# Performance work log

Measured on AMD Instinct MI355X. Metric: run time of the kernel, lower is better.

The kernel has to match this reference:

```python
import jax, jax.numpy as jnp
import numpy as np

N_VARS = 16
BATCH = 16
SEQ = 512
P = N_VARS * (N_VARS - 1)  # ordered pairs i != j


def setup_inputs() -> dict:
    key = jax.random.key(0)
    ks = jax.random.split(key, 12)
    n = N_VARS

    def w(k, shape, fan_in):
        return jax.random.normal(k, shape, dtype=jnp.float32) / np.sqrt(fan_in)

    z = lambda *s: jnp.zeros(s, jnp.float32)
    return {
        'data': jax.random.normal(ks[0], (BATCH, SEQ, n), dtype=jnp.float32),
        # structure learner: n*n -> 256 -> 128 -> n*n (dropout skipped / eval mode)
        'Ws1': w(ks[1], (n * n, 256), n * n), 'bs1': z(256),
        'Ws2': w(ks[2], (256, 128), 256), 'bs2': z(128),
        'Ws3': w(ks[3], (128, n * n), 128), 'bs3': z(n * n),
        # per-variable causal mechanisms (stacked): (n-1) -> 128 -> 64 -> 1
        'Wm1': w(ks[4], (n, n - 1, 128), n - 1), 'bm1': z(n, 128),
        'Wm2': w(ks[5], (n, 128, 64), 128), 'bm2': z(n, 64),
        'Wm3': w(ks[6], (n, 64), 64), 'bm3': z(n),
        # per-pair independence tests (stacked): 2 -> 32 -> 1, sigmoid
        'Wt1': w(ks[7], (P, 2, 32), 2), 'bt1': z(P, 32),
        'Wt2': w(ks[8], (P, 32), 32), 'bt2': z(P),
    }


def reference(data, Ws1, bs1, Ws2, bs2, Ws3, bs3,
              Wm1, bm1, Wm2, bm2, Wm3, bm3,
              Wt1, bt1, Wt2, bt2):
    B, S, n = data.shape
    N = B * S
    flat = data.reshape(N, n)  # [N, n] all samples

    # ---- correlations of batch-averaged series (vectorized corrcoef) ----
    avg = data.mean(axis=0)                    # [S, n]
    xc = avg - avg.mean(axis=0, keepdims=True)
    cov = xc.T @ xc                            # [n, n]
    std = jnp.sqrt(jnp.clip(jnp.diag(cov), 0.0))
    denom = std[:, None] * std[None, :]
    corr = jnp.abs(jnp.where(denom > 0, cov / jnp.where(denom > 0, denom, 1.0), 0.0))
    corr = corr * (1.0 - jnp.eye(n, dtype=corr.dtype))  # zero diagonal (i != j only)

    # ---- structure learner MLP -> sigmoid -> strict upper-tri DAG mask ----
    h = jax.nn.relu(corr.reshape(1, -1) @ Ws1 + bs1)
    h = jax.nn.relu(h @ Ws2 + bs2)
    adj = jax.nn.sigmoid(h @ Ws3 + bs3).reshape(n, n)
    adj = jnp.triu(adj, 1)

    # ---- causal mechanisms: gather-parents -> per-var MLP -> scatter ----
    idx = np.stack([[j for j in range(n) if j != v] for v in range(n)])  # [n, n-1]
    pmask = adj > 0.5
    parent_mask = pmask[idx, np.arange(n)[:, None]].astype(flat.dtype)   # [n, n-1]
    inp = flat[:, idx] * parent_mask[None]                               # [N, n, n-1]
    h1 = jax.nn.relu(jnp.einsum('nvp,vph->nvh', inp, Wm1) + bm1)         # [N, n, 128]
    h2 = jax.nn.relu(jnp.einsum('nvh,vhk->nvk', h1, Wm2) + bm2)          # [N, n, 64]
    mech = jnp.einsum('nvk,vk->nv', h2, Wm3) + bm3                       # [N, n]
    has_parents = parent_mask.sum(axis=1) > 0                            # [n]
    predictions = jnp.where(has_parents[None, :], mech, flat).reshape(B, S, n)

    # ---- batched per-pair independence tests ----
    pairs = np.array([(i, j) for i in range(n) for j in range(n) if i != j])
    pi, pj = pairs[:, 0], pairs[:, 1]
    X = jnp.stack([flat[:, pi], flat[:, pj]], axis=-1)                   # [N, P, 2]
    ht = jax.nn.relu(jnp.einsum('npc,pch->nph', X, Wt1) + bt1)           # [N, P, 32]
    s = jax.nn.sigmoid(jnp.einsum('nph,ph->np', ht, Wt2) + bt2).mean(axis=0)  # [P]
    scores = jnp.zeros((n, n), flat.dtype).at[pi, pj].set(s)

    return adj, predictions, scores
```

## Files before the change

### kernel.cpp

```cpp
#include <hip/hip_runtime.h>
#include <hip/hip_bf16.h>


typedef __attribute__((ext_vector_type(8))) short bf16x8;
typedef __attribute__((ext_vector_type(4))) short bf16x4;
typedef __attribute__((ext_vector_type(4))) float f32x4;

#define DEV __device__ __forceinline__
DEV short f2bf(float f){ __hip_bfloat16 h = __float2bfloat16(f); short s; __builtin_memcpy(&s,&h,2); return s; }

struct GraphSm {
    float avT[16 * 532];
    float part[512];
    float cov[256];
    float corr[256];
    float h1[256];
    float h2[128];
    float adj[256];
    float m[16];
    float stdv[16];
};
struct MechSm {
    short W2T[64 * 136];
    short H1[8][16 * 136];
    float W1[16 * 128];
    float B1[128];
    float B2[64];
    float W3[64];
};
struct PairSm {
    float w0[32], w1[32], bb[32], w2[32];
    float red[512];
    float b2s;
};
union SmU { GraphSm g; MechSm m; PairSm p; };

__global__ void __launch_bounds__(512, 2) k_fused(
    const float* __restrict__ data,
    const float* __restrict__ Ws1, const float* __restrict__ bs1,
    const float* __restrict__ Ws2, const float* __restrict__ bs2,
    const float* __restrict__ Ws3, const float* __restrict__ bs3,
    const float* __restrict__ Wm1, const float* __restrict__ bm1,
    const float* __restrict__ Wm2, const float* __restrict__ bm2,
    const float* __restrict__ Wm3, const float* __restrict__ bm3,
    const float* __restrict__ Wt1, const float* __restrict__ bt1,
    const float* __restrict__ Wt2, const float* __restrict__ bt2,
    float* __restrict__ out)
{
    __shared__ __align__(16) SmU sm;
    __shared__ float pm_s[16];
    __shared__ float hp_s;
    int tid = threadIdx.x, bid = blockIdx.x;

    if (bid >= 64) {
        int p = bid - 64;
        int i = p / 15, jr = p % 15;
        int j = jr + (jr >= i ? 1 : 0);
        if (tid < 32) {
            sm.p.w0[tid] = Wt1[p*64 + tid];
            sm.p.w1[tid] = Wt1[p*64 + 32 + tid];
            sm.p.bb[tid] = bt1[p*32 + tid];
            sm.p.w2[tid] = Wt2[p*32 + tid];
        }
        if (tid == 0) sm.p.b2s = bt2[p];
        __syncthreads();
        float b2sv = sm.p.b2s;
        float acc = 0.f;
        for (int it = 0; it < 16; ++it) {
            int s = it*512 + tid;
            float xa = data[s*16 + i];
            float xb = data[s*16 + j];
            float za = 0.f, zb = 0.f;
            #pragma unroll
            for (int h = 0; h < 32; h += 2) {
                float t1 = fmaf(xa, sm.p.w0[h],   fmaf(xb, sm.p.w1[h],   sm.p.bb[h]));
                za = fmaf(fmaxf(t1, 0.f), sm.p.w2[h],   za);
                float t2 = fmaf(xa, sm.p.w0[h+1], fmaf(xb, sm.p.w1[h+1], sm.p.bb[h+1]));
                zb = fmaf(fmaxf(t2, 0.f), sm.p.w2[h+1], zb);
            }
            float z = b2sv + za + zb;
            acc += __builtin_amdgcn_rcpf(1.f + __expf(-z));
        }
        sm.p.red[tid] = acc;
        __syncthreads();
        for (int off = 256; off > 0; off >>= 1) {
            if (tid < off) sm.p.red[tid] += sm.p.red[tid + off];
            __syncthreads();
        }
        if (tid == 0) out[256 + 131072 + i*16 + j] = sm.p.red[0] * (1.f/8192.f);
        return;
    }

    int v = bid >> 2, chunk = bid & 3;
    int gs0 = chunk * 2048;

    {
        int vb = (tid & 3) * 4, sg = tid >> 2;
        for (int k = 0; k < 4; ++k) {
            int s = sg + k*128;
            float ax=0.f, ay=0.f, az=0.f, aw=0.f;
            #pragma unroll
            for (int b = 0; b < 16; ++b) {
                float4 d4 = *(const float4*)&data[b*8192 + s*16 + vb];
                ax += d4.x; ay += d4.y; az += d4.z; aw += d4.w;
            }
            sm.g.avT[(vb+0)*532 + s] = ax * 0.0625f;
            sm.g.avT[(vb+1)*532 + s] = ay * 0.0625f;
            sm.g.avT[(vb+2)*532 + s] = az * 0.0625f;
            sm.g.avT[(vb+3)*532 + s] = aw * 0.0625f;
        }
    }
    __syncthreads();
    if (tid < 128) {
        int vv = tid >> 3, sgm = tid & 7;
        const float* rp = &sm.g.avT[vv*532 + sgm*64];
        float a0=0.f, a1=0.f, a2=0.f, a3=0.f;
        for (int s = 0; s < 64; s += 4) {
            float4 fa = *(const float4*)&rp[s];
            a0 += fa.x; a1 += fa.y; a2 += fa.z; a3 += fa.w;
        }
        sm.g.part[tid] = (a0+a1)+(a2+a3);
    }
    __syncthreads();
    if (tid < 16) {
        float ms = 0.f;
        #pragma unroll
        for (int q = 0; q < 8; ++q) ms += sm.g.part[tid*8 + q];
        sm.g.m[tid] = ms * (1.f/512.f);
    }
    __syncthreads();
    {
        int t = tid & 255, hh = tid >> 8;
        int ci = t >> 4, cj = t & 15;
        const float* pi_ = &sm.g.avT[ci*532 + hh*256];
        const float* pj_ = &sm.g.avT[cj*532 + hh*256];
        float a0=0.f, a1=0.f, a2=0.f, a3=0.f;
        for (int s = 0; s < 256; s += 4) {
            float4 fa = *(const float4*)&pi_[s];
            float4 fb = *(const float4*)&pj_[s];
            a0 = fmaf(fa.x, fb.x, a0); a1 = fmaf(fa.y, fb.y, a1);
            a2 = fmaf(fa.z, fb.z, a2); a3 = fmaf(fa.w, fb.w, a3);
        }
        sm.g.part[tid] = (a0+a1)+(a2+a3);
    }
    __syncthreads();
    if (tid < 256) {
        int ci = tid >> 4, cj = tid & 15;
        sm.g.cov[tid] = sm.g.part[tid] + sm.g.part[256 + tid]
                      - 512.f * sm.g.m[ci] * sm.g.m[cj];
    }
    __syncthreads();
    if (tid < 16) sm.g.stdv[tid] = sqrtf(fmaxf(sm.g.cov[tid*17], 0.f));
    __syncthreads();
    if (tid < 256) {
        int ci = tid >> 4, cj = tid & 15;
        float den = sm.g.stdv[ci] * sm.g.stdv[cj];
        sm.g.corr[tid] = (den > 0.f && ci != cj) ? fabsf(sm.g.cov[tid]/den) : 0.f;
    }
    __syncthreads();
    {
        int t = tid & 255, half = tid >> 8;
        const float* W1p = Ws1 + half*128*256;
        const float* cp  = sm.g.corr + half*128;
        float a0=0.f, a1=0.f, a2=0.f, a3=0.f;
        #pragma unroll 8
        for (int i = 0; i < 128; i += 4) {
            a0 = fmaf(cp[i  ], W1p[(i  )*256 + t], a0);
            a1 = fmaf(cp[i+1], W1p[(i+1)*256 + t], a1);
            a2 = fmaf(cp[i+2], W1p[(i+2)*256 + t], a2);
            a3 = fmaf(cp[i+3], W1p[(i+3)*256 + t], a3);
        }
        sm.g.part[half*256 + t] = (a0+a1)+(a2+a3);
    }
    __syncthreads();
    if (tid < 256) sm.g.h1[tid] = fmaxf(sm.g.part[tid] + sm.g.part[256+tid] + bs1[tid], 0.f);
    __syncthreads();
    {
        int t = tid & 127, qq = tid >> 7;
        const float* W2p = Ws2 + qq*64*128;
        const float* h1p = sm.g.h1 + qq*64;
        float a0=0.f, a1=0.f, a2=0.f, a3=0.f;
        #pragma unroll 4
        for (int i = 0; i < 64; i += 4) {
            a0 = fmaf(h1p[i  ], W2p[(i  )*128 + t], a0);
            a1 = fmaf(h1p[i+1], W2p[(i+1)*128 + t], a1);
            a2 = fmaf(h1p[i+2], W2p[(i+2)*128 + t], a2);
            a3 = fmaf(h1p[i+3], W2p[(i+3)*128 + t], a3);
        }
        sm.g.part[qq*128 + t] = (a0+a1)+(a2+a3);
    }
    __syncthreads();
    if (tid < 128)
        sm.g.h2[tid] = fmaxf(sm.g.part[tid] + sm.g.part[128+tid] + sm.g.part[256+tid]
                             + sm.g.part[384+tid] + bs2[tid], 0.f);
    __syncthreads();
    {
        int t = tid & 255, half = tid >> 8;
        const float* W3p = Ws3 + half*64*256;
        const float* h2p = sm.g.h2 + half*64;
        float a0=0.f, a1=0.f, a2=0.f, a3=0.f;
        #pragma unroll 4
        for (int i = 0; i < 64; i += 4) {
            a0 = fmaf(h2p[i  ], W3p[(i  )*256 + t], a0);
            a1 = fmaf(h2p[i+1], W3p[(i+1)*256 + t], a1);
            a2 = fmaf(h2p[i+2], W3p[(i+2)*256 + t], a2);
            a3 = fmaf(h2p[i+3], W3p[(i+3)*256 + t], a3);
        }
        sm.g.part[half*256 + t] = (a0+a1)+(a2+a3);
    }
    __syncthreads();
    if (tid < 256) {
        float z = sm.g.part[tid] + sm.g.part[256 + tid] + bs3[tid];
        float a = 1.f / (1.f + expf(-z));
        int r = tid >> 4, cc = tid & 15;
        float adjv = (r < cc) ? a : 0.f;
        sm.g.adj[tid] = adjv;
        if (bid == 0) out[tid] = adjv;
    }
    __syncthreads();
    if (tid < 15) {
        int jj = tid + (tid >= v ? 1 : 0);
        pm_s[tid] = (sm.g.adj[jj*16 + v] > 0.5f) ? 1.f : 0.f;
    }
    if (bid == 0 && tid >= 16 && tid < 32)
        out[256 + 131072 + (tid-16)*17] = 0.f;
    __syncthreads();
    if (tid == 0) {
        float s = 0.f;
        #pragma unroll
        for (int pr = 0; pr < 15; ++pr) s += pm_s[pr];
        hp_s = (s > 0.f) ? 1.f : 0.f;
    }
    __syncthreads();

    for (int e = tid; e < 2048; e += 512) {
        int k = e >> 7, h = e & 127;
        float val = 0.f;
        if (k != v) {
            int p = k - (k > v ? 1 : 0);
            val = Wm1[v*1920 + p*128 + h] * pm_s[p];
        }
        sm.m.W1[e] = val;
    }
    for (int e = tid; e < 8192; e += 512) {
        int h = e >> 6, jj2 = e & 63;
        sm.m.W2T[jj2*136 + h] = f2bf(Wm2[v*8192 + e]);
    }
    if (tid < 128) sm.m.B1[tid] = bm1[v*128 + tid];
    else if (tid < 192) sm.m.B2[tid - 128] = bm2[v*64 + tid - 128];
    else if (tid < 256) sm.m.W3[tid - 192] = Wm3[v*64 + tid - 192];
    __syncthreads();

    int lane = tid & 63, wid = tid >> 6;
    int c = lane & 15, q = lane >> 4;
    float hp = hp_s;
    float bm3v = bm3[v];

    bf16x8 a1f[8];
    #pragma unroll
    for (int ht = 0; ht < 8; ++ht) {
        #pragma unroll
        for (int jj = 0; jj < 8; ++jj) {
            int k = q*8 + jj;
            float w = (k < 16) ? sm.m.W1[k*128 + ht*16 + c] : 0.f;
            a1f[ht][jj] = f2bf(w);
        }
    }
    bf16x8 b2r[16];
    #pragma unroll
    for (int jt = 0; jt < 4; ++jt)
        #pragma unroll
        for (int ks = 0; ks < 4; ++ks)
            b2r[jt*4 + ks] = *(const bf16x8*)&sm.m.W2T[(jt*16 + c)*136 + ks*32 + q*8];
    float w3c[4], b2c[4];
    #pragma unroll
    for (int jt = 0; jt < 4; ++jt) { w3c[jt] = sm.m.W3[jt*16 + c]; b2c[jt] = sm.m.B2[jt*16 + c]; }

    short* h1buf = sm.m.H1[wid];

    for (int stl = 0; stl < 16; ++stl) {
        int st = wid*16 + stl;
        bf16x8 xb;
        #pragma unroll
        for (int i2 = 0; i2 < 8; ++i2) xb[i2] = 0;
        if (q < 2) {
            const float* xp = &data[(gs0 + st*16 + c)*16 + q*8];
            float4 u0 = *(const float4*)xp;
            float4 u1 = *(const float4*)(xp + 4);
            xb[0] = f2bf(u0.x); xb[1] = f2bf(u0.y);
            xb[2] = f2bf(u0.z); xb[3] = f2bf(u0.w);
            xb[4] = f2bf(u1.x); xb[5] = f2bf(u1.y);
            xb[6] = f2bf(u1.z); xb[7] = f2bf(u1.w);
        }
        f32x4 c1[8];
        #pragma unroll
        for (int ht = 0; ht < 8; ++ht) c1[ht] = *(const f32x4*)&sm.m.B1[ht*16 + q*4];
        #pragma unroll
        for (int ht = 0; ht < 8; ++ht)
            c1[ht] = __builtin_amdgcn_mfma_f32_16x16x32_bf16(a1f[ht], xb, c1[ht], 0, 0, 0);
        #pragma unroll
        for (int ht = 0; ht < 8; ++ht) {
            bf16x4 pk;
            #pragma unroll
            for (int r = 0; r < 4; ++r) pk[r] = f2bf(fmaxf(c1[ht][r], 0.f));
            *(bf16x4*)&h1buf[c*136 + ht*16 + q*4] = pk;
        }
        f32x4 c2[4];
        #pragma unroll
        for (int jt = 0; jt < 4; ++jt) {
            float bi = b2c[jt];
            c2[jt] = (f32x4){bi, bi, bi, bi};
        }
        #pragma unroll
        for (int ks = 0; ks < 4; ++ks) {
            bf16x8 a2 = *(const bf16x8*)&h1buf[c*136 + ks*32 + q*8];
            #pragma unroll
            for (int jt = 0; jt < 4; ++jt)
                c2[jt] = __builtin_amdgcn_mfma_f32_16x16x32_bf16(a2, b2r[jt*4 + ks], c2[jt], 0, 0, 0);
        }
        float part[4];
        #pragma unroll
        for (int r = 0; r < 4; ++r) part[r] = 0.f;
        #pragma unroll
        for (int jt = 0; jt < 4; ++jt)
            #pragma unroll
            for (int r = 0; r < 4; ++r)
                part[r] = fmaf(fmaxf(c2[jt][r], 0.f), w3c[jt], part[r]);
        #pragma unroll
        for (int off = 1; off < 16; off <<= 1)
            #pragma unroll
            for (int r = 0; r < 4; ++r)
                part[r] += __shfl_xor(part[r], off, 16);
        if (c == 0) {
            #pragma unroll
            for (int r = 0; r < 4; ++r) {
                int s_loc = st*16 + q*4 + r;
                float mech = part[r] + bm3v;
                float xv = data[(gs0 + s_loc)*16 + v];
                out[256 + (gs0 + s_loc)*16 + v] = (hp != 0.f) ? mech : xv;
            }
        }
    }
}

extern "C" void kernel_launch(void* const* d_in, const int* in_sizes, int n_in,
                              void* d_out, int out_size, void* d_ws, size_t ws_size,
                              hipStream_t stream)
{
    const float* data = (const float*)d_in[0];
    const float* Ws1  = (const float*)d_in[1];
    const float* bs1  = (const float*)d_in[2];
    const float* Ws2  = (const float*)d_in[3];
    const float* bs2  = (const float*)d_in[4];
    const float* Ws3  = (const float*)d_in[5];
    const float* bs3  = (const float*)d_in[6];
    const float* Wm1  = (const float*)d_in[7];
    const float* bm1  = (const float*)d_in[8];
    const float* Wm2  = (const float*)d_in[9];
    const float* bm2  = (const float*)d_in[10];
    const float* Wm3  = (const float*)d_in[11];
    const float* bm3  = (const float*)d_in[12];
    const float* Wt1  = (const float*)d_in[13];
    const float* bt1  = (const float*)d_in[14];
    const float* Wt2  = (const float*)d_in[15];
    const float* bt2  = (const float*)d_in[16];
    float* out = (float*)d_out;
    (void)d_ws; (void)ws_size; (void)in_sizes; (void)n_in; (void)out_size;

    hipLaunchKernelGGL(k_fused, dim3(304), dim3(512), 0, stream,
                       data, Ws1, bs1, Ws2, bs2, Ws3, bs3,
                       Wm1, bm1, Wm2, bm2, Wm3, bm3,
                       Wt1, bt1, Wt2, bt2, out);
}
```

Measured before the change: 125.5 us.

## Double mechanism blocks, prefetch inputs, and restructure structure-MLP matvecs

Splits each variable's mechanism work across eight blocks instead of four, growing the grid, and raises the launch-bounds occupancy hint. It adds one-iteration software prefetch of data loads in both the pair-test and mechanism loops. It also rewrites the three structure-learner matvecs to use float4 weight loads with a wider split-K reduction through shared memory. The extra blocks each recompute the redundant graph/MLP prologue, and the tighter register bound may cause spills.

```diff
diff --git a/kernel.cpp b/kernel.cpp
--- a/kernel.cpp
+++ b/kernel.cpp
@@ -35,7 +35,7 @@
 };
 union SmU { GraphSm g; MechSm m; PairSm p; };
 
-__global__ void __launch_bounds__(512, 2) k_fused(
+__global__ void __launch_bounds__(512, 4) k_fused(
     const float* __restrict__ data,
     const float* __restrict__ Ws1, const float* __restrict__ bs1,
     const float* __restrict__ Ws2, const float* __restrict__ bs2,
@@ -52,8 +52,8 @@
     __shared__ float hp_s;
     int tid = threadIdx.x, bid = blockIdx.x;
 
-    if (bid >= 64) {
-        int p = bid - 64;
+    if (bid >= 128) {
+        int p = bid - 128;
         int i = p / 15, jr = p % 15;
         int j = jr + (jr >= i ? 1 : 0);
         if (tid < 32) {
@@ -66,10 +66,15 @@
         __syncthreads();
         float b2sv = sm.p.b2s;
         float acc = 0.f;
+        float nxa = data[tid*16 + i];
+        float nxb = data[tid*16 + j];
         for (int it = 0; it < 16; ++it) {
-            int s = it*512 + tid;
-            float xa = data[s*16 + i];
-            float xb = data[s*16 + j];
+            float xa = nxa, xb = nxb;
+            if (it < 15) {
+                int sn = (it+1)*512 + tid;
+                nxa = data[sn*16 + i];
+                nxb = data[sn*16 + j];
+            }
             float za = 0.f, zb = 0.f;
             #pragma unroll
             for (int h = 0; h < 32; h += 2) {
@@ -91,8 +96,8 @@
         return;
     }
 
-    int v = bid >> 2, chunk = bid & 3;
-    int gs0 = chunk * 2048;
+    int v = bid >> 3, chunk = bid & 7;
+    int gs0 = chunk * 1024;
 
     {
         int vb = (tid & 3) * 4, sg = tid >> 2;
@@ -135,6 +140,7 @@
         const float* pi_ = &sm.g.avT[ci*532 + hh*256];
         const float* pj_ = &sm.g.avT[cj*532 + hh*256];
         float a0=0.f, a1=0.f, a2=0.f, a3=0.f;
+        #pragma unroll 8
         for (int s = 0; s < 256; s += 4) {
             float4 fa = *(const float4*)&pi_[s];
             float4 fb = *(const float4*)&pj_[s];
@@ -158,59 +164,81 @@
         sm.g.corr[tid] = (den > 0.f && ci != cj) ? fabsf(sm.g.cov[tid]/den) : 0.f;
     }
     __syncthreads();
-    {
-        int t = tid & 255, half = tid >> 8;
-        const float* W1p = Ws1 + half*128*256;
-        const float* cp  = sm.g.corr + half*128;
-        float a0=0.f, a1=0.f, a2=0.f, a3=0.f;
+
+    float* red2 = sm.g.avT;
+
+    {
+        int o4 = tid & 63, ks = tid >> 6;
+        const float* W1p = Ws1 + ks*32*256 + o4*4;
+        const float* cp  = sm.g.corr + ks*32;
+        float ax=0.f, ay=0.f, az=0.f, aw=0.f;
+        float bx=0.f, by=0.f, bz=0.f, bw=0.f;
         #pragma unroll 8
-        for (int i = 0; i < 128; i += 4) {
-            a0 = fmaf(cp[i  ], W1p[(i  )*256 + t], a0);
-            a1 = fmaf(cp[i+1], W1p[(i+1)*256 + t], a1);
-            a2 = fmaf(cp[i+2], W1p[(i+2)*256 + t], a2);
-            a3 = fmaf(cp[i+3], W1p[(i+3)*256 + t], a3);
-        }
-        sm.g.part[half*256 + t] = (a0+a1)+(a2+a3);
-    }
-    __syncthreads();
-    if (tid < 256) sm.g.h1[tid] = fmaxf(sm.g.part[tid] + sm.g.part[256+tid] + bs1[tid], 0.f);
-    __syncthreads();
-    {
-        int t = tid & 127, qq = tid >> 7;
-        const float* W2p = Ws2 + qq*64*128;
-        const float* h1p = sm.g.h1 + qq*64;
-        float a0=0.f, a1=0.f, a2=0.f, a3=0.f;
-        #pragma unroll 4
-        for (int i = 0; i < 64; i += 4) {
-            a0 = fmaf(h1p[i  ], W2p[(i  )*128 + t], a0);
-            a1 = fmaf(h1p[i+1], W2p[(i+1)*128 + t], a1);
-            a2 = fmaf(h1p[i+2], W2p[(i+2)*128 + t], a2);
-            a3 = fmaf(h1p[i+3], W2p[(i+3)*128 + t], a3);
-        }
-        sm.g.part[qq*128 + t] = (a0+a1)+(a2+a3);
-    }
-    __syncthreads();
-    if (tid < 128)
-        sm.g.h2[tid] = fmaxf(sm.g.part[tid] + sm.g.part[128+tid] + sm.g.part[256+tid]
-                             + sm.g.part[384+tid] + bs2[tid], 0.f);
-    __syncthreads();
-    {
-        int t = tid & 255, half = tid >> 8;
-        const float* W3p = Ws3 + half*64*256;
-        const float* h2p = sm.g.h2 + half*64;
-        float a0=0.f, a1=0.f, a2=0.f, a3=0.f;
-        #pragma unroll 4
-        for (int i = 0; i < 64; i += 4) {
-            a0 = fmaf(h2p[i  ], W3p[(i  )*256 + t], a0);
-            a1 = fmaf(h2p[i+1], W3p[(i+1)*256 + t], a1);
-            a2 = fmaf(h2p[i+2], W3p[(i+2)*256 + t], a2);
-            a3 = fmaf(h2p[i+3], W3p[(i+3)*256 + t], a3);
-        }
-        sm.g.part[half*256 + t] = (a0+a1)+(a2+a3);
+        for (int i = 0; i < 32; i += 2) {
+            float4 w0 = *(const float4*)&W1p[(i  )*256];
+            float4 w1 = *(const float4*)&W1p[(i+1)*256];
+            float c0 = cp[i], c1 = cp[i+1];
+            ax=fmaf(c0,w0.x,ax); ay=fmaf(c0,w0.y,ay); az=fmaf(c0,w0.z,az); aw=fmaf(c0,w0.w,aw);
+            bx=fmaf(c1,w1.x,bx); by=fmaf(c1,w1.y,by); bz=fmaf(c1,w1.z,bz); bw=fmaf(c1,w1.w,bw);
+        }
+        float4 r4; r4.x=ax+bx; r4.y=ay+by; r4.z=az+bz; r4.w=aw+bw;
+        *(float4*)&red2[ks*256 + o4*4] = r4;
     }
     __syncthreads();
     if (tid < 256) {
-        float z = sm.g.part[tid] + sm.g.part[256 + tid] + bs3[tid];
+        float s = bs1[tid];
+        #pragma unroll
+        for (int k2 = 0; k2 < 8; ++k2) s += red2[k2*256 + tid];
+        sm.g.h1[tid] = fmaxf(s, 0.f);
+    }
+    __syncthreads();
+    {
+        int o4 = tid & 31, ks = tid >> 5;
+        const float* W2p = Ws2 + ks*16*128 + o4*4;
+        const float* cp  = sm.g.h1 + ks*16;
+        float ax=0.f, ay=0.f, az=0.f, aw=0.f;
+        float bx=0.f, by=0.f, bz=0.f, bw=0.f;
+        #pragma unroll
+        for (int i = 0; i < 16; i += 2) {
+            float4 w0 = *(const float4*)&W2p[(i  )*128];
+            float4 w1 = *(const float4*)&W2p[(i+1)*128];
+            float c0 = cp[i], c1 = cp[i+1];
+            ax=fmaf(c0,w0.x,ax); ay=fmaf(c0,w0.y,ay); az=fmaf(c0,w0.z,az); aw=fmaf(c0,w0.w,aw);
+            bx=fmaf(c1,w1.x,bx); by=fmaf(c1,w1.y,by); bz=fmaf(c1,w1.z,bz); bw=fmaf(c1,w1.w,bw);
+        }
+        float4 r4; r4.x=ax+bx; r4.y=ay+by; r4.z=az+bz; r4.w=aw+bw;
+        *(float4*)&red2[ks*128 + o4*4] = r4;
+    }
+    __syncthreads();
+    if (tid < 128) {
+        float s = bs2[tid];
+        #pragma unroll
+        for (int k2 = 0; k2 < 16; ++k2) s += red2[k2*128 + tid];
+        sm.g.h2[tid] = fmaxf(s, 0.f);
+    }
+    __syncthreads();
+    {
+        int o4 = tid & 63, ks = tid >> 6;
+        const float* W3p = Ws3 + ks*16*256 + o4*4;
+        const float* cp  = sm.g.h2 + ks*16;
+        float ax=0.f, ay=0.f, az=0.f, aw=0.f;
+        float bx=0.f, by=0.f, bz=0.f, bw=0.f;
+        #pragma unroll
+        for (int i = 0; i < 16; i += 2) {
+            float4 w0 = *(const float4*)&W3p[(i  )*256];
+            float4 w1 = *(const float4*)&W3p[(i+1)*256];
+            float c0 = cp[i], c1 = cp[i+1];
+            ax=fmaf(c0,w0.x,ax); ay=fmaf(c0,w0.y,ay); az=fmaf(c0,w0.z,az); aw=fmaf(c0,w0.w,aw);
+            bx=fmaf(c1,w1.x,bx); by=fmaf(c1,w1.y,by); bz=fmaf(c1,w1.z,bz); bw=fmaf(c1,w1.w,bw);
+        }
+        float4 r4; r4.x=ax+bx; r4.y=ay+by; r4.z=az+bz; r4.w=aw+bw;
+        *(float4*)&red2[ks*256 + o4*4] = r4;
+    }
+    __syncthreads();
+    if (tid < 256) {
+        float z = bs3[tid];
+        #pragma unroll
+        for (int k2 = 0; k2 < 8; ++k2) z += red2[k2*256 + tid];
         float a = 1.f / (1.f + expf(-z));
         int r = tid >> 4, cc = tid & 15;
         float adjv = (r < cc) ? a : 0.f;
@@ -277,16 +305,30 @@
     for (int jt = 0; jt < 4; ++jt) { w3c[jt] = sm.m.W3[jt*16 + c]; b2c[jt] = sm.m.B2[jt*16 + c]; }
 
     short* h1buf = sm.m.H1[wid];
-
-    for (int stl = 0; stl < 16; ++stl) {
-        int st = wid*16 + stl;
+    bool act = (q < 2);
+
+    float4 u0c, u1c;
+    {
+        int st0 = wid*8;
+        if (act) {
+            const float* xp = &data[(gs0 + st0*16 + c)*16 + q*8];
+            u0c = *(const float4*)xp;
+            u1c = *(const float4*)(xp + 4);
+        }
+    }
+
+    for (int stl = 0; stl < 8; ++stl) {
+        int st = wid*8 + stl;
+        float4 u0 = u0c, u1 = u1c;
+        if (stl < 7 && act) {
+            const float* xp = &data[(gs0 + (st+1)*16 + c)*16 + q*8];
+            u0c = *(const float4*)xp;
+            u1c = *(const float4*)(xp + 4);
+        }
         bf16x8 xb;
         #pragma unroll
         for (int i2 = 0; i2 < 8; ++i2) xb[i2] = 0;
-        if (q < 2) {
-            const float* xp = &data[(gs0 + st*16 + c)*16 + q*8];
-            float4 u0 = *(const float4*)xp;
-            float4 u1 = *(const float4*)(xp + 4);
+        if (act) {
             xb[0] = f2bf(u0.x); xb[1] = f2bf(u0.y);
             xb[2] = f2bf(u0.z); xb[3] = f2bf(u0.w);
             xb[4] = f2bf(u1.x); xb[5] = f2bf(u1.y);
@@ -367,7 +409,7 @@
     float* out = (float*)d_out;
     (void)d_ws; (void)ws_size; (void)in_sizes; (void)n_in; (void)out_size;
 
-    hipLaunchKernelGGL(k_fused, dim3(304), dim3(512), 0, stream,
+    hipLaunchKernelGGL(k_fused, dim3(368), dim3(512), 0, stream,
                        data, Ws1, bs1, Ws2, bs2, Ws3, bs3,
                        Wm1, bm1, Wm2, bm2, Wm3, bm3,
                        Wt1, bt1, Wt2, bt2, out);
```

Result: slower. 151.6 us (+20.8%).
